# Kernel optimization log

Hardware: AMD Instinct MI355X
Metric: run time of the kernel (lower is better)

## Reference

```python
import jax, jax.numpy as jnp
import numpy as np

N, C, L = 64, 3, 4096
K, S = 128, 64  # num_shapelets, shapelets_size


def setup_inputs() -> dict:
    key = jax.random.key(0)
    kx, ks = jax.random.split(key)
    x = jax.random.normal(kx, (N, C, L), dtype=jnp.float32)
    shapelets = jax.random.normal(ks, (C, K, S), dtype=jnp.float32)
    return {"x": x, "shapelets": shapelets}


def _min_euclid(x, shapelets):
    # x: (N, C, L); shapelets: (C, K, S)
    # Torch does unfold -> cdist -> min over windows -> min over channels.
    # We compute ||x_w - s||^2 = ||x_w||^2 + ||s||^2 - 2<x_w, s> with sliding
    # dot products via grouped 1-D conv (avoids materializing the unfold).
    C_, K_, S_ = shapelets.shape
    n = x.shape[0]
    filt = shapelets.reshape(C_ * K_, 1, S_)  # OIW, grouped by channel
    dots = jax.lax.conv_general_dilated(
        x, filt, window_strides=(1,), padding="VALID",
        dimension_numbers=("NCW", "OIW", "NCW"),
        feature_group_count=C_)                      # (N, C*K, W)
    ones = jnp.ones((C_, 1, S_), x.dtype)
    x2 = jax.lax.conv_general_dilated(
        x * x, ones, window_strides=(1,), padding="VALID",
        dimension_numbers=("NCW", "OIW", "NCW"),
        feature_group_count=C_)                      # (N, C, W) sliding ||x_w||^2
    W_ = dots.shape[-1]
    dots = dots.reshape(n, C_, K_, W_)               # (N, C, K, W)
    s2 = jnp.sum(shapelets * shapelets, axis=-1)     # (C, K)
    d2 = x2[:, :, None, :] + s2[None, :, :, None] - 2.0 * dots
    d = jnp.sqrt(jnp.maximum(d2, 0.0))               # Euclidean distance (N,C,K,W)
    d = jnp.min(d, axis=3)                           # min over windows -> (N, C, K)
    d = jnp.min(d, axis=1)                           # min over channels -> (N, K)
    return d[:, None, :]                             # (N, 1, K)


def reference(x, shapelets):
    return _min_euclid(x, shapelets)
```

## Files before the change

### kernel.cpp

```cpp
#include <hip/hip_runtime.h>
#include <hip/hip_bf16.h>

#define NN 64
#define CC 3
#define LL 4096
#define SS 64
#define KK 128
#define WW 4033
#define BLKN 8

typedef __attribute__((ext_vector_type(8))) short v8s;
typedef __attribute__((ext_vector_type(4))) float v4f;

#define WS_CNT_OFF 32768
#define WS_HS2_OFF 33024
#define WS_SHB_OFF 34560
#define WS_HX2_OFF 131072

__device__ __forceinline__ unsigned bf16_rne(float f) {
    unsigned u = __float_as_uint(f);
    return (u + 0x7FFFu + ((u >> 16) & 1u)) >> 16;
}

__global__ __launch_bounds__(256) void me_prep(
        const float* __restrict__ x,
        const float* __restrict__ shp,
        unsigned* __restrict__ d2g,
        unsigned* __restrict__ cnt,
        float* __restrict__ hs2g,
        uint4* __restrict__ shb,
        float* __restrict__ hx2g) {
    const int b = blockIdx.x, t = threadIdx.x;
    if (b < NN * CC) {
        const int n = b / 3, c = b - n * 3;
        __shared__ float P[LL];
        __shared__ float wtot[4];
        const int lane = t & 63, wave = t >> 6;
        const float* xc = x + ((size_t)n * CC + c) * LL;
        const int base = t * 16;
        float q[16];
        {
            float4 A0 = *(const float4*)(xc + base);
            float4 A1 = *(const float4*)(xc + base + 4);
            float4 A2 = *(const float4*)(xc + base + 8);
            float4 A3 = *(const float4*)(xc + base + 12);
            q[0]=A0.x; q[1]=A0.y; q[2]=A0.z;  q[3]=A0.w;
            q[4]=A1.x; q[5]=A1.y; q[6]=A1.z;  q[7]=A1.w;
            q[8]=A2.x; q[9]=A2.y; q[10]=A2.z; q[11]=A2.w;
            q[12]=A3.x;q[13]=A3.y;q[14]=A3.z; q[15]=A3.w;
        }
        float run = 0.f;
        #pragma unroll
        for (int i = 0; i < 16; ++i) { run += q[i] * q[i]; q[i] = run; }
        float sc = run;
        #pragma unroll
        for (int d = 1; d < 64; d <<= 1) {
            float u = __shfl_up(sc, d, 64);
            if (lane >= d) sc += u;
        }
        if (lane == 63) wtot[wave] = sc;
        __syncthreads();
        float excl = sc - run;
        for (int w2 = 0; w2 < wave; ++w2) excl += wtot[w2];
        #pragma unroll
        for (int i = 0; i < 16; ++i) q[i] += excl;
        *(float4*)(P + base)      = make_float4(q[0], q[1], q[2], q[3]);
        *(float4*)(P + base + 4)  = make_float4(q[4], q[5], q[6], q[7]);
        *(float4*)(P + base + 8)  = make_float4(q[8], q[9], q[10], q[11]);
        *(float4*)(P + base + 12) = make_float4(q[12], q[13], q[14], q[15]);
        __syncthreads();
        float* dst = hx2g + ((size_t)n * CC + c) * LL;
        #pragma unroll
        for (int i = 0; i < 16; ++i) {
            int w = base + i;
            float o = -1e30f;
            if (w < WW) {
                float I1 = P[w + 63];
                float I0 = (w > 0) ? P[w - 1] : 0.f;
                o = -0.5f * (I1 - I0);
            }
            dst[w] = o;
        }
    } else {
        int tid = (b - NN * CC) * 256 + t;
        if (tid < NN * KK) d2g[tid] = 0x7F800000u;
        if (tid < NN) cnt[tid] = 0u;
        if (tid < CC * KK) {
            const float* r = shp + tid * SS;
            float a = 0.f;
            #pragma unroll 8
            for (int s = 0; s < SS; ++s) a += r[s] * r[s];
            hs2g[tid] = -0.5f * a;
        }
        if (tid < CC * 1024) {
            int c   = tid >> 10;
            int r   = tid & 1023;
            int nt  = r >> 7;
            int scb = (r >> 6) & 1;
            int l   = r & 63;
            int row  = nt * 16 + (l & 15);
            int koff = scb * 32 + (l >> 4) * 8;
            const float* s = shp + ((size_t)(c * KK + row)) * SS + koff;
            float4 f0 = *(const float4*)s;
            float4 f1 = *(const float4*)(s + 4);
            uint4 o;
            o.x = (bf16_rne(f0.y) << 16) | bf16_rne(f0.x);
            o.y = (bf16_rne(f0.w) << 16) | bf16_rne(f0.z);
            o.z = (bf16_rne(f1.y) << 16) | bf16_rne(f1.x);
            o.w = (bf16_rne(f1.w) << 16) | bf16_rne(f1.z);
            shb[tid] = o;
        }
    }
}

__global__ __launch_bounds__(256, 2) void me_main(
        const float* __restrict__ x,
        const ushort* __restrict__ shb_g,
        const float* __restrict__ hs2g,
        const float* __restrict__ hx2g,
        unsigned* __restrict__ d2g,
        unsigned* __restrict__ cnt,
        float* __restrict__ out) {

    __shared__ __align__(16) ushort shb[CC * 8192];
    __shared__ __align__(8) ushort xs2[2][2][CC][320];
    __shared__ unsigned red[KK];
    __shared__ int lastflag;

    const int b    = blockIdx.x;
    const int n    = b >> 3;
    const int tg   = b & 7;
    const int t    = threadIdx.x;
    const int lane = t & 63, wave = t >> 6;
    const int quad = lane >> 4, col = lane & 15;
    const int wbase = wave * 64;

    if (t < KK) red[t] = 0x7F800000u;

    {
        typedef __attribute__((address_space(1))) const uint4 gu4;
        typedef __attribute__((address_space(3))) uint4 lu4;
        const uint4* gbase = (const uint4*)shb_g;
        #pragma unroll
        for (int it = 0; it < 12; ++it) {
            const uint4* gp = gbase + it * 256 + t;
            uint4* lp = (uint4*)shb + (it * 256 + wave * 64);
            __builtin_amdgcn_global_load_lds((gu4*)gp, (lu4*)lp, 16, 0, 0);
        }
    }

    float hsv[CC][8];
    #pragma unroll
    for (int c = 0; c < CC; ++c)
        #pragma unroll
        for (int nt = 0; nt < 8; ++nt)
            hsv[c][nt] = hs2g[c * KK + nt * 16 + col];

    const float* xb   = x + (size_t)n * (CC * LL);
    const float* hx2b = hx2g + (size_t)n * (CC * LL);

    float rmax[8];
    #pragma unroll
    for (int nt = 0; nt < 8; ++nt) rmax[nt] = -3.4e38f;

    for (int it = 0; it < 2; ++it) {
        const int buf = it;
        const int w0  = tg * 512 + it * 256;

        if (t < 240) {
            int c = t / 80, q = t - c * 80;
            int idx = q * 4, gi = w0 + idx;
            float4 v;
            if (gi + 3 < LL) v = *(const float4*)(xb + c * LL + gi);
            else {
                v.x = (gi     < LL) ? xb[c * LL + gi]     : 0.f;
                v.y = (gi + 1 < LL) ? xb[c * LL + gi + 1] : 0.f;
                v.z = (gi + 2 < LL) ? xb[c * LL + gi + 2] : 0.f;
                v.w = (gi + 3 < LL) ? xb[c * LL + gi + 3] : 0.f;
            }
            unsigned h0 = bf16_rne(v.x), h1 = bf16_rne(v.y);
            unsigned h2 = bf16_rne(v.z), h3 = bf16_rne(v.w);
            uint2 p0; p0.x = h0 | (h1 << 16); p0.y = h2 | (h3 << 16);
            *(uint2*)&xs2[buf][0][c][idx] = p0;
            if (idx > 0) xs2[buf][1][c][idx - 1] = (ushort)h0;
            *(uint*)&xs2[buf][1][c][idx] = h1 | (h2 << 16);
            xs2[buf][1][c][idx + 2] = (ushort)h3;
        }
        __syncthreads();

        #pragma unroll
        for (int c = 0; c < CC; ++c) {
            const float* hp = hx2b + c * LL + w0 + wbase + quad * 4;
            v4f hxv[4];
            #pragma unroll
            for (int mt = 0; mt < 4; ++mt) hxv[mt] = *(const v4f*)(hp + mt * 16);
            v8s af[4][2];
            #pragma unroll
            for (int mt = 0; mt < 4; ++mt)
                #pragma unroll
                for (int sc = 0; sc < 2; ++sc) {
                    int e0 = wbase + mt * 16 + col + sc * 32 + quad * 8;
                    int p  = col & 1;
                    const uint* ap = (const uint*)&xs2[buf][p][c][e0 - p];
                    union { v8s v; uint u[4]; } au;
                    au.u[0] = ap[0]; au.u[1] = ap[1];
                    au.u[2] = ap[2]; au.u[3] = ap[3];
                    af[mt][sc] = au.v;
                }
            #pragma unroll
            for (int g = 0; g < 2; ++g) {
                v4f acc[4][4];
                #pragma unroll
                for (int nt2 = 0; nt2 < 4; ++nt2) {
                    float h = hsv[c][g * 4 + nt2];
                    v4f a = {h, h, h, h};
                    #pragma unroll
                    for (int mt = 0; mt < 4; ++mt) acc[nt2][mt] = a;
                }
                #pragma unroll
                for (int sc = 0; sc < 2; ++sc)
                    #pragma unroll
                    for (int nt2 = 0; nt2 < 4; ++nt2) {
                        int nt = g * 4 + nt2;
                        v8s bfr = *(const v8s*)(shb + (((c * 8 + nt) * 2 + sc) * 64 + lane) * 8);
                        #pragma unroll
                        for (int mt = 0; mt < 4; ++mt)
                            acc[nt2][mt] = __builtin_amdgcn_mfma_f32_16x16x32_bf16(
                                af[mt][sc], bfr, acc[nt2][mt], 0, 0, 0);
                    }
                #pragma unroll
                for (int nt2 = 0; nt2 < 4; ++nt2) {
                    float m = -3.4e38f;
                    #pragma unroll
                    for (int mt = 0; mt < 4; ++mt) {
                        v4f a = acc[nt2][mt];
                        #pragma unroll
                        for (int r = 0; r < 4; ++r)
                            m = fmaxf(m, a[r] + hxv[mt][r]);
                    }
                    rmax[g * 4 + nt2] = fmaxf(rmax[g * 4 + nt2], m);
                }
            }
        }
    }

    #pragma unroll
    for (int nt = 0; nt < 8; ++nt) {
        float v = rmax[nt];
        v = fmaxf(v, __shfl_xor(v, 16, 64));
        v = fmaxf(v, __shfl_xor(v, 32, 64));
        rmax[nt] = v;
    }
    if (quad == 0) {
        #pragma unroll
        for (int nt = 0; nt < 8; ++nt) {
            float d2 = fmaxf(-2.f * rmax[nt], 0.f);
            atomicMin(&red[nt * 16 + col], __float_as_uint(d2));
        }
    }
    __syncthreads();
    if (t < KK) atomicMin(&d2g[n * KK + t], red[t]);

    __syncthreads();
    if (t == 0) {
        unsigned old = atomicAdd(&cnt[n], 1u);
        lastflag = (old == BLKN - 1) ? 1 : 0;
    }
    __syncthreads();
    if (lastflag && t < KK) {
        unsigned bits = atomicMin(&d2g[n * KK + t], 0x7F800000u);
        out[n * KK + t] = sqrtf(__uint_as_float(bits));
    }
}

extern "C" void kernel_launch(void* const* d_in, const int* in_sizes, int n_in,
                              void* d_out, int out_size, void* d_ws, size_t ws_size,
                              hipStream_t stream) {
    const float* x   = (const float*)d_in[0];
    const float* shp = (const float*)d_in[1];
    unsigned* d2g  = (unsigned*)d_ws;
    unsigned* cnt  = (unsigned*)((char*)d_ws + WS_CNT_OFF);
    float*    hs2g = (float*)((char*)d_ws + WS_HS2_OFF);
    uint4*    shb  = (uint4*)((char*)d_ws + WS_SHB_OFF);
    float*    hx2g = (float*)((char*)d_ws + WS_HX2_OFF);
    float* out = (float*)d_out;

    hipLaunchKernelGGL(me_prep, dim3(NN * CC + 32), dim3(256), 0, stream,
                       x, shp, d2g, cnt, hs2g, shb, hx2g);
    hipLaunchKernelGGL(me_main, dim3(NN * BLKN), dim3(256), 0, stream,
                       x, (const ushort*)shb, hs2g, hx2g, d2g, cnt, out);
}
```

Measured before the change: 75.86 us.

## Fuse prep into main kernel and replace atomic reduction with finalize kernel

Drops the separate prep kernel. Each main block now converts the shapelets to bf16 and computes their squared norms itself, and it computes the sliding window energies of x locally with an in-wave prefix scan held in LDS. The atomic min reduction and last-block counter are replaced by per-block partial minima in workspace, which a small finalize kernel reduces and square-roots. This removes a launch and a global round-trip for the window energies, but every block now redoes the shapelet conversion and adds extra barriers.

```diff
diff --git a/kernel.cpp b/kernel.cpp
--- a/kernel.cpp
+++ b/kernel.cpp
@@ -1,5 +1,4 @@
 #include <hip/hip_runtime.h>
-#include <hip/hip_bf16.h>
 
 #define NN 64
 #define CC 3
@@ -12,120 +11,20 @@
 typedef __attribute__((ext_vector_type(8))) short v8s;
 typedef __attribute__((ext_vector_type(4))) float v4f;
 
-#define WS_CNT_OFF 32768
-#define WS_HS2_OFF 33024
-#define WS_SHB_OFF 34560
-#define WS_HX2_OFF 131072
-
 __device__ __forceinline__ unsigned bf16_rne(float f) {
     unsigned u = __float_as_uint(f);
     return (u + 0x7FFFu + ((u >> 16) & 1u)) >> 16;
 }
 
-__global__ __launch_bounds__(256) void me_prep(
+__global__ __launch_bounds__(256, 2) void me_main(
         const float* __restrict__ x,
         const float* __restrict__ shp,
-        unsigned* __restrict__ d2g,
-        unsigned* __restrict__ cnt,
-        float* __restrict__ hs2g,
-        uint4* __restrict__ shb,
-        float* __restrict__ hx2g) {
-    const int b = blockIdx.x, t = threadIdx.x;
-    if (b < NN * CC) {
-        const int n = b / 3, c = b - n * 3;
-        __shared__ float P[LL];
-        __shared__ float wtot[4];
-        const int lane = t & 63, wave = t >> 6;
-        const float* xc = x + ((size_t)n * CC + c) * LL;
-        const int base = t * 16;
-        float q[16];
-        {
-            float4 A0 = *(const float4*)(xc + base);
-            float4 A1 = *(const float4*)(xc + base + 4);
-            float4 A2 = *(const float4*)(xc + base + 8);
-            float4 A3 = *(const float4*)(xc + base + 12);
-            q[0]=A0.x; q[1]=A0.y; q[2]=A0.z;  q[3]=A0.w;
-            q[4]=A1.x; q[5]=A1.y; q[6]=A1.z;  q[7]=A1.w;
-            q[8]=A2.x; q[9]=A2.y; q[10]=A2.z; q[11]=A2.w;
-            q[12]=A3.x;q[13]=A3.y;q[14]=A3.z; q[15]=A3.w;
-        }
-        float run = 0.f;
-        #pragma unroll
-        for (int i = 0; i < 16; ++i) { run += q[i] * q[i]; q[i] = run; }
-        float sc = run;
-        #pragma unroll
-        for (int d = 1; d < 64; d <<= 1) {
-            float u = __shfl_up(sc, d, 64);
-            if (lane >= d) sc += u;
-        }
-        if (lane == 63) wtot[wave] = sc;
-        __syncthreads();
-        float excl = sc - run;
-        for (int w2 = 0; w2 < wave; ++w2) excl += wtot[w2];
-        #pragma unroll
-        for (int i = 0; i < 16; ++i) q[i] += excl;
-        *(float4*)(P + base)      = make_float4(q[0], q[1], q[2], q[3]);
-        *(float4*)(P + base + 4)  = make_float4(q[4], q[5], q[6], q[7]);
-        *(float4*)(P + base + 8)  = make_float4(q[8], q[9], q[10], q[11]);
-        *(float4*)(P + base + 12) = make_float4(q[12], q[13], q[14], q[15]);
-        __syncthreads();
-        float* dst = hx2g + ((size_t)n * CC + c) * LL;
-        #pragma unroll
-        for (int i = 0; i < 16; ++i) {
-            int w = base + i;
-            float o = -1e30f;
-            if (w < WW) {
-                float I1 = P[w + 63];
-                float I0 = (w > 0) ? P[w - 1] : 0.f;
-                o = -0.5f * (I1 - I0);
-            }
-            dst[w] = o;
-        }
-    } else {
-        int tid = (b - NN * CC) * 256 + t;
-        if (tid < NN * KK) d2g[tid] = 0x7F800000u;
-        if (tid < NN) cnt[tid] = 0u;
-        if (tid < CC * KK) {
-            const float* r = shp + tid * SS;
-            float a = 0.f;
-            #pragma unroll 8
-            for (int s = 0; s < SS; ++s) a += r[s] * r[s];
-            hs2g[tid] = -0.5f * a;
-        }
-        if (tid < CC * 1024) {
-            int c   = tid >> 10;
-            int r   = tid & 1023;
-            int nt  = r >> 7;
-            int scb = (r >> 6) & 1;
-            int l   = r & 63;
-            int row  = nt * 16 + (l & 15);
-            int koff = scb * 32 + (l >> 4) * 8;
-            const float* s = shp + ((size_t)(c * KK + row)) * SS + koff;
-            float4 f0 = *(const float4*)s;
-            float4 f1 = *(const float4*)(s + 4);
-            uint4 o;
-            o.x = (bf16_rne(f0.y) << 16) | bf16_rne(f0.x);
-            o.y = (bf16_rne(f0.w) << 16) | bf16_rne(f0.z);
-            o.z = (bf16_rne(f1.y) << 16) | bf16_rne(f1.x);
-            o.w = (bf16_rne(f1.w) << 16) | bf16_rne(f1.z);
-            shb[tid] = o;
-        }
-    }
-}
-
-__global__ __launch_bounds__(256, 2) void me_main(
-        const float* __restrict__ x,
-        const ushort* __restrict__ shb_g,
-        const float* __restrict__ hs2g,
-        const float* __restrict__ hx2g,
-        unsigned* __restrict__ d2g,
-        unsigned* __restrict__ cnt,
-        float* __restrict__ out) {
+        float* __restrict__ part) {
 
     __shared__ __align__(16) ushort shb[CC * 8192];
-    __shared__ __align__(8) ushort xs2[2][2][CC][320];
-    __shared__ unsigned red[KK];
-    __shared__ int lastflag;
+    __shared__ __align__(8)  ushort xs2[2][2][CC][320];
+    __shared__ __align__(16) float  Ps[CC][320];
+    __shared__ __align__(16) float  hx[CC][256];
 
     const int b    = blockIdx.x;
     const int n    = b >> 3;
@@ -135,29 +34,48 @@
     const int quad = lane >> 4, col = lane & 15;
     const int wbase = wave * 64;
 
-    if (t < KK) red[t] = 0x7F800000u;
-
-    {
-        typedef __attribute__((address_space(1))) const uint4 gu4;
-        typedef __attribute__((address_space(3))) uint4 lu4;
-        const uint4* gbase = (const uint4*)shb_g;
-        #pragma unroll
-        for (int it = 0; it < 12; ++it) {
-            const uint4* gp = gbase + it * 256 + t;
-            uint4* lp = (uint4*)shb + (it * 256 + wave * 64);
-            __builtin_amdgcn_global_load_lds((gu4*)gp, (lu4*)lp, 16, 0, 0);
-        }
-    }
+    float* hs = &hx[0][0];
+
+    #pragma unroll
+    for (int i = 0; i < 12; ++i) {
+        int tid  = i * 256 + t;
+        int c    = tid >> 10;
+        int r    = tid & 1023;
+        int nt   = r >> 7;
+        int scb  = (r >> 6) & 1;
+        int l    = r & 63;
+        int row  = nt * 16 + (l & 15);
+        int koff = scb * 32 + (l >> 4) * 8;
+        const float* s = shp + (size_t)(c * KK + row) * SS + koff;
+        float4 f0 = *(const float4*)s;
+        float4 f1 = *(const float4*)(s + 4);
+        uint4 o;
+        o.x = (bf16_rne(f0.y) << 16) | bf16_rne(f0.x);
+        o.y = (bf16_rne(f0.w) << 16) | bf16_rne(f0.z);
+        o.z = (bf16_rne(f1.y) << 16) | bf16_rne(f1.x);
+        o.w = (bf16_rne(f1.w) << 16) | bf16_rne(f1.z);
+        ((uint4*)shb)[tid] = o;
+    }
+    for (int tid = t; tid < CC * KK; tid += 256) {
+        const float4* r4 = (const float4*)(shp + (size_t)tid * SS);
+        float a = 0.f;
+        #pragma unroll
+        for (int i = 0; i < 16; ++i) {
+            float4 v = r4[i];
+            a += v.x * v.x + v.y * v.y + v.z * v.z + v.w * v.w;
+        }
+        hs[tid] = -0.5f * a;
+    }
+    __syncthreads();
 
     float hsv[CC][8];
     #pragma unroll
     for (int c = 0; c < CC; ++c)
         #pragma unroll
         for (int nt = 0; nt < 8; ++nt)
-            hsv[c][nt] = hs2g[c * KK + nt * 16 + col];
-
-    const float* xb   = x + (size_t)n * (CC * LL);
-    const float* hx2b = hx2g + (size_t)n * (CC * LL);
+            hsv[c][nt] = hs[c * KK + nt * 16 + col];
+
+    const float* xb = x + (size_t)n * (CC * LL);
 
     float rmax[8];
     #pragma unroll
@@ -186,14 +104,49 @@
             *(uint*)&xs2[buf][1][c][idx] = h1 | (h2 << 16);
             xs2[buf][1][c][idx + 2] = (ushort)h3;
         }
+        if (wave < CC) {
+            const float* xp = xb + wave * LL + w0;
+            float qq[5];
+            #pragma unroll
+            for (int i = 0; i < 5; ++i) {
+                int idx = lane * 5 + i;
+                float v = (w0 + idx < LL) ? xp[idx] : 0.f;
+                qq[i] = v * v;
+            }
+            float run = 0.f;
+            #pragma unroll
+            for (int i = 0; i < 5; ++i) { run += qq[i]; qq[i] = run; }
+            float sc = run;
+            #pragma unroll
+            for (int d = 1; d < 64; d <<= 1) {
+                float u = __shfl_up(sc, d, 64);
+                if (lane >= d) sc += u;
+            }
+            float excl = sc - run;
+            #pragma unroll
+            for (int i = 0; i < 5; ++i) Ps[wave][lane * 5 + i] = qq[i] + excl;
+        }
         __syncthreads();
 
+        {
+            int w = t;
+            #pragma unroll
+            for (int c = 0; c < CC; ++c) {
+                float I1 = Ps[c][w + 63];
+                float I0 = (w > 0) ? Ps[c][w - 1] : 0.f;
+                float o = -0.5f * (I1 - I0);
+                if (w0 + w >= WW) o = -1e30f;
+                hx[c][w] = o;
+            }
+        }
+        __syncthreads();
+
         #pragma unroll
         for (int c = 0; c < CC; ++c) {
-            const float* hp = hx2b + c * LL + w0 + wbase + quad * 4;
             v4f hxv[4];
             #pragma unroll
-            for (int mt = 0; mt < 4; ++mt) hxv[mt] = *(const v4f*)(hp + mt * 16);
+            for (int mt = 0; mt < 4; ++mt)
+                hxv[mt] = *(const v4f*)&hx[c][wbase + mt * 16 + quad * 4];
             v8s af[4][2];
             #pragma unroll
             for (int mt = 0; mt < 4; ++mt)
@@ -244,6 +197,7 @@
         }
     }
 
+    float (*wred)[KK] = (float (*)[KK])&Ps[0][0];
     #pragma unroll
     for (int nt = 0; nt < 8; ++nt) {
         float v = rmax[nt];
@@ -253,24 +207,26 @@
     }
     if (quad == 0) {
         #pragma unroll
-        for (int nt = 0; nt < 8; ++nt) {
-            float d2 = fmaxf(-2.f * rmax[nt], 0.f);
-            atomicMin(&red[nt * 16 + col], __float_as_uint(d2));
-        }
+        for (int nt = 0; nt < 8; ++nt)
+            wred[wave][nt * 16 + col] = fmaxf(-2.f * rmax[nt], 0.f);
     }
     __syncthreads();
-    if (t < KK) atomicMin(&d2g[n * KK + t], red[t]);
-
-    __syncthreads();
-    if (t == 0) {
-        unsigned old = atomicAdd(&cnt[n], 1u);
-        lastflag = (old == BLKN - 1) ? 1 : 0;
-    }
-    __syncthreads();
-    if (lastflag && t < KK) {
-        unsigned bits = atomicMin(&d2g[n * KK + t], 0x7F800000u);
-        out[n * KK + t] = sqrtf(__uint_as_float(bits));
-    }
+    if (t < KK) {
+        float m = fminf(fminf(wred[0][t], wred[1][t]),
+                        fminf(wred[2][t], wred[3][t]));
+        part[b * KK + t] = m;
+    }
+}
+
+__global__ __launch_bounds__(128) void me_fin(
+        const float* __restrict__ part,
+        float* __restrict__ out) {
+    const int n = blockIdx.x, k = threadIdx.x;
+    float m = part[(size_t)(n * BLKN) * KK + k];
+    #pragma unroll
+    for (int i = 1; i < BLKN; ++i)
+        m = fminf(m, part[(size_t)(n * BLKN + i) * KK + k]);
+    out[n * KK + k] = sqrtf(m);
 }
 
 extern "C" void kernel_launch(void* const* d_in, const int* in_sizes, int n_in,
@@ -278,15 +234,10 @@
                               hipStream_t stream) {
     const float* x   = (const float*)d_in[0];
     const float* shp = (const float*)d_in[1];
-    unsigned* d2g  = (unsigned*)d_ws;
-    unsigned* cnt  = (unsigned*)((char*)d_ws + WS_CNT_OFF);
-    float*    hs2g = (float*)((char*)d_ws + WS_HS2_OFF);
-    uint4*    shb  = (uint4*)((char*)d_ws + WS_SHB_OFF);
-    float*    hx2g = (float*)((char*)d_ws + WS_HX2_OFF);
-    float* out = (float*)d_out;
-
-    hipLaunchKernelGGL(me_prep, dim3(NN * CC + 32), dim3(256), 0, stream,
-                       x, shp, d2g, cnt, hs2g, shb, hx2g);
+    float* part = (float*)d_ws;
+    float* out  = (float*)d_out;
+
     hipLaunchKernelGGL(me_main, dim3(NN * BLKN), dim3(256), 0, stream,
-                       x, (const ushort*)shb, hs2g, hx2g, d2g, cnt, out);
-}
+                       x, shp, part);
+    hipLaunchKernelGGL(me_fin, dim3(NN), dim3(KK), 0, stream, part, out);
+}
```

New measurement: 80.48 us. 1.06x slower.

## Fuse sliding window squared-norm computation into main kernel via per-tile LDS prefix scan

Applied to the files above, without the earlier changes.

Removes the per-(n,c) prefix-sum pass from the prep kernel and instead computes the sliding ||x_w||^2 inside the main kernel for each 256-window tile. Three waves each load 320 samples, scan them with wave shuffles into LDS, and a second pass forms the windowed differences into a small LDS array. This drops the global hx2 write/read round trip and shrinks the prep kernel to 32 blocks. In exchange the main kernel does extra scalar global loads, an extra barrier per tile and uses more LDS, which could reduce occupancy.

```diff
diff --git a/kernel.cpp b/kernel.cpp
--- a/kernel.cpp
+++ b/kernel.cpp
@@ -1,5 +1,4 @@
 #include <hip/hip_runtime.h>
-#include <hip/hip_bf16.h>
 
 #define NN 64
 #define CC 3
@@ -15,7 +14,6 @@
 #define WS_CNT_OFF 32768
 #define WS_HS2_OFF 33024
 #define WS_SHB_OFF 34560
-#define WS_HX2_OFF 131072
 
 __device__ __forceinline__ unsigned bf16_rne(float f) {
     unsigned u = __float_as_uint(f);
@@ -23,93 +21,41 @@
 }
 
 __global__ __launch_bounds__(256) void me_prep(
-        const float* __restrict__ x,
         const float* __restrict__ shp,
         unsigned* __restrict__ d2g,
         unsigned* __restrict__ cnt,
         float* __restrict__ hs2g,
-        uint4* __restrict__ shb,
-        float* __restrict__ hx2g) {
-    const int b = blockIdx.x, t = threadIdx.x;
-    if (b < NN * CC) {
-        const int n = b / 3, c = b - n * 3;
-        __shared__ float P[LL];
-        __shared__ float wtot[4];
-        const int lane = t & 63, wave = t >> 6;
-        const float* xc = x + ((size_t)n * CC + c) * LL;
-        const int base = t * 16;
-        float q[16];
-        {
-            float4 A0 = *(const float4*)(xc + base);
-            float4 A1 = *(const float4*)(xc + base + 4);
-            float4 A2 = *(const float4*)(xc + base + 8);
-            float4 A3 = *(const float4*)(xc + base + 12);
-            q[0]=A0.x; q[1]=A0.y; q[2]=A0.z;  q[3]=A0.w;
-            q[4]=A1.x; q[5]=A1.y; q[6]=A1.z;  q[7]=A1.w;
-            q[8]=A2.x; q[9]=A2.y; q[10]=A2.z; q[11]=A2.w;
-            q[12]=A3.x;q[13]=A3.y;q[14]=A3.z; q[15]=A3.w;
-        }
-        float run = 0.f;
-        #pragma unroll
-        for (int i = 0; i < 16; ++i) { run += q[i] * q[i]; q[i] = run; }
-        float sc = run;
-        #pragma unroll
-        for (int d = 1; d < 64; d <<= 1) {
-            float u = __shfl_up(sc, d, 64);
-            if (lane >= d) sc += u;
-        }
-        if (lane == 63) wtot[wave] = sc;
-        __syncthreads();
-        float excl = sc - run;
-        for (int w2 = 0; w2 < wave; ++w2) excl += wtot[w2];
-        #pragma unroll
-        for (int i = 0; i < 16; ++i) q[i] += excl;
-        *(float4*)(P + base)      = make_float4(q[0], q[1], q[2], q[3]);
-        *(float4*)(P + base + 4)  = make_float4(q[4], q[5], q[6], q[7]);
-        *(float4*)(P + base + 8)  = make_float4(q[8], q[9], q[10], q[11]);
-        *(float4*)(P + base + 12) = make_float4(q[12], q[13], q[14], q[15]);
-        __syncthreads();
-        float* dst = hx2g + ((size_t)n * CC + c) * LL;
+        uint4* __restrict__ shb) {
+    const int tid = blockIdx.x * 256 + threadIdx.x;
+    d2g[tid] = 0x7F800000u;
+    if (tid < NN) cnt[tid] = 0u;
+    if (tid < CC * KK) {
+        const float4* r4 = (const float4*)(shp + (size_t)tid * SS);
+        float a = 0.f;
         #pragma unroll
         for (int i = 0; i < 16; ++i) {
-            int w = base + i;
-            float o = -1e30f;
-            if (w < WW) {
-                float I1 = P[w + 63];
-                float I0 = (w > 0) ? P[w - 1] : 0.f;
-                o = -0.5f * (I1 - I0);
-            }
-            dst[w] = o;
-        }
-    } else {
-        int tid = (b - NN * CC) * 256 + t;
-        if (tid < NN * KK) d2g[tid] = 0x7F800000u;
-        if (tid < NN) cnt[tid] = 0u;
-        if (tid < CC * KK) {
-            const float* r = shp + tid * SS;
-            float a = 0.f;
-            #pragma unroll 8
-            for (int s = 0; s < SS; ++s) a += r[s] * r[s];
-            hs2g[tid] = -0.5f * a;
-        }
-        if (tid < CC * 1024) {
-            int c   = tid >> 10;
-            int r   = tid & 1023;
-            int nt  = r >> 7;
-            int scb = (r >> 6) & 1;
-            int l   = r & 63;
-            int row  = nt * 16 + (l & 15);
-            int koff = scb * 32 + (l >> 4) * 8;
-            const float* s = shp + ((size_t)(c * KK + row)) * SS + koff;
-            float4 f0 = *(const float4*)s;
-            float4 f1 = *(const float4*)(s + 4);
-            uint4 o;
-            o.x = (bf16_rne(f0.y) << 16) | bf16_rne(f0.x);
-            o.y = (bf16_rne(f0.w) << 16) | bf16_rne(f0.z);
-            o.z = (bf16_rne(f1.y) << 16) | bf16_rne(f1.x);
-            o.w = (bf16_rne(f1.w) << 16) | bf16_rne(f1.z);
-            shb[tid] = o;
-        }
+            float4 v = r4[i];
+            a += v.x * v.x + v.y * v.y + v.z * v.z + v.w * v.w;
+        }
+        hs2g[tid] = -0.5f * a;
+    }
+    if (tid < CC * 1024) {
+        int c   = tid >> 10;
+        int r   = tid & 1023;
+        int nt  = r >> 7;
+        int scb = (r >> 6) & 1;
+        int l   = r & 63;
+        int row  = nt * 16 + (l & 15);
+        int koff = scb * 32 + (l >> 4) * 8;
+        const float* s = shp + ((size_t)(c * KK + row)) * SS + koff;
+        float4 f0 = *(const float4*)s;
+        float4 f1 = *(const float4*)(s + 4);
+        uint4 o;
+        o.x = (bf16_rne(f0.y) << 16) | bf16_rne(f0.x);
+        o.y = (bf16_rne(f0.w) << 16) | bf16_rne(f0.z);
+        o.z = (bf16_rne(f1.y) << 16) | bf16_rne(f1.x);
+        o.w = (bf16_rne(f1.w) << 16) | bf16_rne(f1.z);
+        shb[tid] = o;
     }
 }
 
@@ -117,13 +63,14 @@
         const float* __restrict__ x,
         const ushort* __restrict__ shb_g,
         const float* __restrict__ hs2g,
-        const float* __restrict__ hx2g,
         unsigned* __restrict__ d2g,
         unsigned* __restrict__ cnt,
         float* __restrict__ out) {
 
     __shared__ __align__(16) ushort shb[CC * 8192];
     __shared__ __align__(8) ushort xs2[2][2][CC][320];
+    __shared__ __align__(16) float Ps[CC][320];
+    __shared__ __align__(16) float hx[CC][256];
     __shared__ unsigned red[KK];
     __shared__ int lastflag;
 
@@ -156,8 +103,7 @@
         for (int nt = 0; nt < 8; ++nt)
             hsv[c][nt] = hs2g[c * KK + nt * 16 + col];
 
-    const float* xb   = x + (size_t)n * (CC * LL);
-    const float* hx2b = hx2g + (size_t)n * (CC * LL);
+    const float* xb = x + (size_t)n * (CC * LL);
 
     float rmax[8];
     #pragma unroll
@@ -186,14 +132,49 @@
             *(uint*)&xs2[buf][1][c][idx] = h1 | (h2 << 16);
             xs2[buf][1][c][idx + 2] = (ushort)h3;
         }
+        if (wave < CC) {
+            const float* xp = xb + wave * LL + w0;
+            float qq[5];
+            #pragma unroll
+            for (int i = 0; i < 5; ++i) {
+                int idx = lane * 5 + i;
+                float v = (w0 + idx < LL) ? xp[idx] : 0.f;
+                qq[i] = v * v;
+            }
+            float run = 0.f;
+            #pragma unroll
+            for (int i = 0; i < 5; ++i) { run += qq[i]; qq[i] = run; }
+            float sc = run;
+            #pragma unroll
+            for (int d = 1; d < 64; d <<= 1) {
+                float u = __shfl_up(sc, d, 64);
+                if (lane >= d) sc += u;
+            }
+            float excl = sc - run;
+            #pragma unroll
+            for (int i = 0; i < 5; ++i) Ps[wave][lane * 5 + i] = qq[i] + excl;
+        }
         __syncthreads();
 
+        {
+            int w = t;
+            #pragma unroll
+            for (int c = 0; c < CC; ++c) {
+                float I1 = Ps[c][w + 63];
+                float I0 = (w > 0) ? Ps[c][w - 1] : 0.f;
+                float o = -0.5f * (I1 - I0);
+                if (w0 + w >= WW) o = -1e30f;
+                hx[c][w] = o;
+            }
+        }
+        __syncthreads();
+
         #pragma unroll
         for (int c = 0; c < CC; ++c) {
-            const float* hp = hx2b + c * LL + w0 + wbase + quad * 4;
             v4f hxv[4];
             #pragma unroll
-            for (int mt = 0; mt < 4; ++mt) hxv[mt] = *(const v4f*)(hp + mt * 16);
+            for (int mt = 0; mt < 4; ++mt)
+                hxv[mt] = *(const v4f*)&hx[c][wbase + mt * 16 + quad * 4];
             v8s af[4][2];
             #pragma unroll
             for (int mt = 0; mt < 4; ++mt)
@@ -282,11 +263,10 @@
     unsigned* cnt  = (unsigned*)((char*)d_ws + WS_CNT_OFF);
     float*    hs2g = (float*)((char*)d_ws + WS_HS2_OFF);
     uint4*    shb  = (uint4*)((char*)d_ws + WS_SHB_OFF);
-    float*    hx2g = (float*)((char*)d_ws + WS_HX2_OFF);
     float* out = (float*)d_out;
 
-    hipLaunchKernelGGL(me_prep, dim3(NN * CC + 32), dim3(256), 0, stream,
-                       x, shp, d2g, cnt, hs2g, shb, hx2g);
+    hipLaunchKernelGGL(me_prep, dim3(32), dim3(256), 0, stream,
+                       shp, d2g, cnt, hs2g, shb);
     hipLaunchKernelGGL(me_main, dim3(NN * BLKN), dim3(256), 0, stream,
-                       x, (const ushort*)shb, hs2g, hx2g, d2g, cnt, out);
-}
+                       x, (const ushort*)shb, hs2g, d2g, cnt, out);
+}
```

Result: no change. 74.45 us (-1.9%).
